# Performance work log

Hardware: AMD Instinct MI355X
Metric: run time of the kernel (lower is better)

The kernel has to match this reference:

```python
import jax, jax.numpy as jnp
import numpy as np
import math

B, N, M, C, H = 8, 2048, 2048, 512, 8
DK = C // H
EPS_LN = 1e-5


def _layernorm(x, g, b):
    mu = jnp.mean(x, axis=-1, keepdims=True)
    var = jnp.var(x, axis=-1, keepdims=True)
    return (x - mu) / jnp.sqrt(var + EPS_LN) * g + b


def setup_inputs() -> dict:
    key = jax.random.key(0)
    ks = jax.random.split(key, 8)
    s = 0.02
    return {
        "cross_x": jax.random.normal(ks[0], (B, N, C), jnp.float32),
        "cross_y": jax.random.normal(ks[1], (B, M, C), jnp.float32),
        "ln_x_g": jnp.ones((C,), jnp.float32),
        "ln_x_b": jnp.zeros((C,), jnp.float32),
        "ln_y_g": jnp.ones((C,), jnp.float32),
        "ln_y_b": jnp.zeros((C,), jnp.float32),
        "Wq": jax.random.normal(ks[2], (C, C), jnp.float32) * s,
        "bq": jnp.zeros((C,), jnp.float32),
        "Wk": jax.random.normal(ks[3], (C, C), jnp.float32) * s,
        "bk": jnp.zeros((C,), jnp.float32),
        "Wv": jax.random.normal(ks[4], (C, C), jnp.float32) * s,
        "bv": jnp.zeros((C,), jnp.float32),
        "Wc": jax.random.normal(ks[5], (C, C), jnp.float32) * s,  # conv1x1 weight [out, in]
        "bc": jnp.zeros((C,), jnp.float32),
        "ln_o_g": jnp.ones((C,), jnp.float32),
        "ln_o_b": jnp.zeros((C,), jnp.float32),
    }


def reference(cross_x, cross_y, ln_x_g, ln_x_b, ln_y_g, ln_y_b,
              Wq, bq, Wk, bk, Wv, bv, Wc, bc, ln_o_g, ln_o_b):
    b, n, c = cross_x.shape
    m = cross_y.shape[1]
    xn = _layernorm(cross_x, ln_x_g, ln_x_b)
    yn = _layernorm(cross_y, ln_y_g, ln_y_b)
    # projections -> [B, H, seq, dk]
    q = (xn @ Wq + bq).reshape(b, n, H, DK).transpose(0, 2, 1, 3)
    k = (yn @ Wk + bk).reshape(b, m, H, DK).transpose(0, 2, 1, 3)
    v = (yn @ Wv + bv).reshape(b, m, H, DK).transpose(0, 2, 1, 3)
    scale = 1.0 / math.sqrt(DK)
    scores = jnp.einsum("bhnd,bhmd->bhnm", q, k) * scale
    attn = jax.nn.softmax(scores, axis=-1)
    # extra renormalization across the HEAD dimension (dim=1)
    attn = attn / (1e-9 + jnp.sum(attn, axis=1, keepdims=True))
    # dropout is identity in eval/reference mode
    o = jnp.einsum("bhnm,bhmd->bhnd", attn, v)
    q_flat = q.transpose(0, 2, 1, 3).reshape(b, n, c)  # [B, N, C]
    o_flat = o.transpose(0, 2, 1, 3).reshape(b, n, c)
    # conv1x1 over channels on (query - x)
    h = (q_flat - o_flat) @ Wc.T + bc
    h = jax.nn.leaky_relu(_layernorm(h, ln_o_g, ln_o_b), negative_slope=0.02)
    return q_flat + h
```

## Files before the change

### kernel.cpp

```cpp
#include <hip/hip_runtime.h>


typedef short bf16x8 __attribute__((ext_vector_type(8)));
typedef float f32x4 __attribute__((ext_vector_type(4)));

#define CS 0.18033688f

#define BARRIER_LG() do { __builtin_amdgcn_sched_barrier(0); \
  asm volatile("s_waitcnt lgkmcnt(0)" ::: "memory"); \
  __builtin_amdgcn_s_barrier(); \
  __builtin_amdgcn_sched_barrier(0); } while(0)

#define VMCNT(N) do { __builtin_amdgcn_sched_barrier(0); \
  asm volatile("s_waitcnt vmcnt(" #N ")" ::: "memory"); \
  __builtin_amdgcn_sched_barrier(0); } while(0)

__device__ inline float b2f(unsigned short u){
  union { unsigned int i; float f; } c; c.i = ((unsigned int)u) << 16; return c.f;
}
__device__ inline unsigned short f2b(float f){
  union { float ff; unsigned int i; } c; c.ff = f;
  unsigned int i = c.i;
  return (unsigned short)((i + 0x7FFFu + ((i >> 16) & 1u)) >> 16);
}
__device__ inline unsigned int cvtpk(float lo, float hi){
  unsigned int r;
  asm("v_cvt_pk_bf16_f32 %0, %1, %2" : "=v"(r) : "v"(lo), "v"(hi));
  return r;
}
__device__ inline float fast_rcp(float x){ return __builtin_amdgcn_rcpf(x); }
__device__ inline f32x4 mfma16(bf16x8 a, bf16x8 b, f32x4 c){
  return __builtin_amdgcn_mfma_f32_16x16x32_bf16(a, b, c, 0, 0, 0);
}
__device__ __forceinline__ void gl16(const unsigned short* g, unsigned short* l){
  __builtin_amdgcn_global_load_lds(
      (const __attribute__((address_space(1))) unsigned int*)g,
      (__attribute__((address_space(3))) unsigned int*)l,
      16, 0, 0);
}

__global__ void detect_dtype(const unsigned int* __restrict__ g, int* __restrict__ flag){
  *flag = (g[0] == 0x3F800000u) ? 1 : 0;
}

__global__ void zero_f32(float* __restrict__ p, int n){
  int i = blockIdx.x * 256 + threadIdx.x;
  if (i < n) p[i] = 0.0f;
}

__global__ void convert_misc(const void* Wc, const void* bq, const void* bk,
    const void* bv, const void* bc, const void* go, const void* bo,
    unsigned short* WcB, unsigned short* bqB, unsigned short* bkB,
    unsigned short* bvB, unsigned short* bcB, unsigned short* goB,
    unsigned short* boB, const int* __restrict__ flag){
  int i = blockIdx.x * 256 + threadIdx.x;
  const void* src; unsigned short* dst; int o;
  if (i < 262144){ src = Wc; dst = WcB; o = i; }
  else {
    int j = i - 262144; int seg = j >> 9; o = j & 511;
    if (seg == 0){ src = bq; dst = bqB; }
    else if (seg == 1){ src = bk; dst = bkB; }
    else if (seg == 2){ src = bv; dst = bvB; }
    else if (seg == 3){ src = bc; dst = bcB; }
    else if (seg == 4){ src = go; dst = goB; }
    else if (seg == 5){ src = bo; dst = boB; }
    else return;
  }
  if (*flag) dst[o] = f2b(((const float*)src)[o]);
  else       dst[o] = ((const unsigned short*)src)[o];
}

__global__ __launch_bounds__(128) void ln_rows(const void* __restrict__ xv,
    const void* __restrict__ gxv, const void* __restrict__ bxv,
    const void* __restrict__ yv, const void* __restrict__ gyv, const void* __restrict__ byv,
    unsigned short* __restrict__ outx, unsigned short* __restrict__ outy,
    const int* __restrict__ flag){
  int row = blockIdx.x & 16383;
  int sel = blockIdx.x >> 14;
  const void* src = sel ? yv : xv;
  const void* gv = sel ? gyv : gxv;
  const void* bv_ = sel ? byv : bxv;
  unsigned short* out = sel ? outy : outx;
  int t = threadIdx.x;
  float v0, v1, v2, v3, g0, g1, g2, g3, bb0, bb1, bb2, bb3;
  if (*flag){
    float4 xf = ((const float4*)((const float*)src + (size_t)row * 512))[t];
    v0 = xf.x; v1 = xf.y; v2 = xf.z; v3 = xf.w;
    float4 gf = ((const float4*)gv)[t];  g0 = gf.x; g1 = gf.y; g2 = gf.z; g3 = gf.w;
    float4 bf = ((const float4*)bv_)[t]; bb0 = bf.x; bb1 = bf.y; bb2 = bf.z; bb3 = bf.w;
  } else {
    ushort4 raw = ((const ushort4*)((const unsigned short*)src + (size_t)row * 512))[t];
    v0 = b2f(raw.x); v1 = b2f(raw.y); v2 = b2f(raw.z); v3 = b2f(raw.w);
    ushort4 gr = ((const ushort4*)gv)[t];  g0 = b2f(gr.x); g1 = b2f(gr.y); g2 = b2f(gr.z); g3 = b2f(gr.w);
    ushort4 br = ((const ushort4*)bv_)[t]; bb0 = b2f(br.x); bb1 = b2f(br.y); bb2 = b2f(br.z); bb3 = b2f(br.w);
  }
  float s = v0 + v1 + v2 + v3;
  float sq = v0*v0 + v1*v1 + v2*v2 + v3*v3;
  #pragma unroll
  for (int off = 32; off; off >>= 1){
    s += __shfl_down(s, off, 64);
    sq += __shfl_down(sq, off, 64);
  }
  __shared__ float red[4];
  if ((t & 63) == 0){ red[(t >> 6)*2] = s; red[(t >> 6)*2 + 1] = sq; }
  __syncthreads();
  s = red[0] + red[2]; sq = red[1] + red[3];
  float mu = s * (1.0f/512.0f);
  float rstd = rsqrtf(sq * (1.0f/512.0f) - mu*mu + 1e-5f);
  ushort4 o;
  o.x = f2b((v0 - mu)*rstd*g0 + bb0);
  o.y = f2b((v1 - mu)*rstd*g1 + bb1);
  o.z = f2b((v2 - mu)*rstd*g2 + bb2);
  o.w = f2b((v3 - mu)*rstd*g3 + bb3);
  ((ushort4*)(out + (size_t)row * 512))[t] = o;
}

__global__ __launch_bounds__(256) void transposeW(const void* __restrict__ wq,
    const void* __restrict__ wk, const void* __restrict__ wv,
    unsigned short* __restrict__ oq, unsigned short* __restrict__ ok,
    unsigned short* __restrict__ ov, const int* __restrict__ flag){
  __shared__ unsigned short tile[32][33];
  const void* in = (blockIdx.z == 0) ? wq : (blockIdx.z == 1) ? wk : wv;
  unsigned short* outp = (blockIdx.z == 0) ? oq : (blockIdx.z == 1) ? ok : ov;
  int k0 = blockIdx.x * 32, j0 = blockIdx.y * 32;
  int t = threadIdx.x;
  int r = t >> 3, c4 = (t & 7) * 4;
  if (*flag){
    float4 v = *(const float4*)((const float*)in + (size_t)(k0 + r) * 512 + j0 + c4);
    tile[r][c4] = f2b(v.x); tile[r][c4+1] = f2b(v.y);
    tile[r][c4+2] = f2b(v.z); tile[r][c4+3] = f2b(v.w);
  } else {
    ushort4 v = *(const ushort4*)((const unsigned short*)in + (size_t)(k0 + r) * 512 + j0 + c4);
    tile[r][c4] = v.x; tile[r][c4+1] = v.y; tile[r][c4+2] = v.z; tile[r][c4+3] = v.w;
  }
  __syncthreads();
  ushort4 o;
  o.x = tile[c4][r]; o.y = tile[c4+1][r]; o.z = tile[c4+2][r]; o.w = tile[c4+3][r];
  *(ushort4*)(outp + (size_t)(j0 + r) * 512 + k0 + c4) = o;
}

template<int OUT_MODE>
__global__ __launch_bounds__(256) void gemm_nt(const unsigned short* __restrict__ A,
    const unsigned short* __restrict__ Bt, const unsigned short* __restrict__ bias,
    void* __restrict__ Cout){
  __shared__ __align__(16) unsigned short As[128*32];
  __shared__ __align__(16) unsigned short Bs[128*32];
  int i0 = blockIdx.x * 128;
  int j0 = blockIdx.y * 128;
  int t = threadIdx.x;
  int w = t >> 6, lane = t & 63;
  int quad = lane >> 4, l15 = lane & 15;
  int wrow = (w >> 1) * 64, wcol = (w & 1) * 64;
  f32x4 acc[4][4];
  #pragma unroll
  for (int a = 0; a < 4; a++)
    #pragma unroll
    for (int b = 0; b < 4; b++)
      acc[a][b] = (f32x4){0.f, 0.f, 0.f, 0.f};

  int ra0 = t >> 2, ca0 = (t & 3) * 8;
  const unsigned short* Ag = A + (size_t)i0 * 512;
  const unsigned short* Bg = Bt + (size_t)j0 * 512;

  for (int kt = 0; kt < 16; kt++){
    int k0 = kt * 32;
    int4 av0 = *(const int4*)(Ag + (size_t)ra0 * 512 + k0 + ca0);
    int4 av1 = *(const int4*)(Ag + (size_t)(64 + ra0) * 512 + k0 + ca0);
    int4 bv0 = *(const int4*)(Bg + (size_t)ra0 * 512 + k0 + ca0);
    int4 bv1 = *(const int4*)(Bg + (size_t)(64 + ra0) * 512 + k0 + ca0);
    __syncthreads();
    ((int4*)As)[t] = av0; ((int4*)As)[t + 256] = av1;
    ((int4*)Bs)[t] = bv0; ((int4*)Bs)[t + 256] = bv1;
    __syncthreads();
    bf16x8 af[4], bfg[4];
    #pragma unroll
    for (int a = 0; a < 4; a++)
      af[a] = *(const bf16x8*)&As[(wrow + a*16 + l15)*32 + quad*8];
    #pragma unroll
    for (int b = 0; b < 4; b++)
      bfg[b] = *(const bf16x8*)&Bs[(wcol + b*16 + l15)*32 + quad*8];
    #pragma unroll
    for (int a = 0; a < 4; a++)
      #pragma unroll
      for (int b = 0; b < 4; b++)
        acc[a][b] = mfma16(af[a], bfg[b], acc[a][b]);
  }

  #pragma unroll
  for (int b = 0; b < 4; b++){
    int gcol = j0 + wcol + b*16 + l15;
    float bv = b2f(bias[gcol]);
    #pragma unroll
    for (int a = 0; a < 4; a++){
      #pragma unroll
      for (int r = 0; r < 4; r++){
        int grow = i0 + wrow + a*16 + quad*4 + r;
        float v = acc[a][b][r] + bv;
        if (OUT_MODE == 0){
          ((unsigned short*)Cout)[(size_t)grow*512 + gcol] = f2b(v);
        } else {
          int bb_ = grow >> 11, m = grow & 2047;
          int h = gcol >> 6, d = gcol & 63;
          ((unsigned short*)Cout)[(((size_t)(bb_*64 + (m >> 5))*512) + h*64 + d)*32
                                  + (m & 31)] = f2b(v);
        }
      }
    }
  }
}

__global__ __launch_bounds__(256) void attn_lsum(const unsigned short* __restrict__ Qm,
    const unsigned short* __restrict__ Km, float* __restrict__ Lsum){
  int wgl = blockIdx.x * 4 + (threadIdx.x >> 6);
  int b = wgl >> 9; int r_ = wgl & 511;
  int ntl = r_ >> 4; int ms = (r_ >> 2) & 3; int hg = r_ & 3;
  int h0 = hg * 2;
  int lane = threadIdx.x & 63, quad = lane >> 4, l15 = lane & 15;
  int n0 = ntl * 64;
  const unsigned short* Kp = Km + ((size_t)(b*2048)) * 512;
  bf16x8 aq[4][2][2];
  #pragma unroll
  for (int ns = 0; ns < 4; ns++)
    #pragma unroll
    for (int hh = 0; hh < 2; hh++)
      #pragma unroll
      for (int ks = 0; ks < 2; ks++)
        aq[ns][hh][ks] = *(const bf16x8*)(Qm + ((size_t)(b*2048 + n0 + ns*16 + l15))*512
                                          + (h0+hh)*64 + ks*32 + quad*8);
  float ls[4][2];
  #pragma unroll
  for (int ns = 0; ns < 4; ns++){ ls[ns][0] = 0.f; ls[ns][1] = 0.f; }
  for (int mt = 0; mt < 16; mt++){
    int m0 = ms*512 + mt*32;
    #pragma unroll
    for (int msub = 0; msub < 2; msub++){
      int mb = m0 + msub*16;
      #pragma unroll
      for (int hh = 0; hh < 2; hh++){
        bf16x8 ak0 = *(const bf16x8*)(Kp + (size_t)(mb + l15)*512 + (h0+hh)*64 + quad*8);
        bf16x8 ak1 = *(const bf16x8*)(Kp + (size_t)(mb + l15)*512 + (h0+hh)*64 + 32 + quad*8);
        #pragma unroll
        for (int ns = 0; ns < 4; ns++){
          f32x4 S = (f32x4){0.f,0.f,0.f,0.f};
          S = mfma16(ak0, aq[ns][hh][0], S);
          S = mfma16(ak1, aq[ns][hh][1], S);
          float e0 = exp2f(S[0]*CS), e1 = exp2f(S[1]*CS);
          float e2 = exp2f(S[2]*CS), e3 = exp2f(S[3]*CS);
          ls[ns][hh] += (e0 + e1) + (e2 + e3);
        }
      }
    }
  }
  #pragma unroll
  for (int ns = 0; ns < 4; ns++)
    #pragma unroll
    for (int hh = 0; hh < 2; hh++){
      float v = ls[ns][hh];
      v += __shfl_xor(v, 16, 64);
      v += __shfl_xor(v, 32, 64);
      ls[ns][hh] = v;
    }
  if (lane < 16){
    #pragma unroll
    for (int ns = 0; ns < 4; ns++)
      #pragma unroll
      for (int hh = 0; hh < 2; hh++)
        atomicAdd(&Lsum[(size_t)(b*8 + h0 + hh)*2048 + n0 + ns*16 + lane], ls[ns][hh]);
  }
}

__global__ __launch_bounds__(1024)
__attribute__((amdgpu_waves_per_eu(4, 4)))
void attn_out(const unsigned short* __restrict__ Qm,
    const unsigned short* __restrict__ Km, const unsigned short* __restrict__ VTm,
    const float* __restrict__ Lsum, unsigned short* __restrict__ DQO){
  __shared__ __align__(16) unsigned short Ks[32*512];
  __shared__ __align__(16) unsigned short Vs[512*32];
  __shared__ __align__(16) float ps[4*4*16*36];
  __shared__ __align__(16) unsigned short pbv[4*4*2*16*40];
  int bid = blockIdx.x;
  int b = bid & 7;
  int ntl = bid >> 3;
  int t = threadIdx.x;
  int w = t >> 6;
  int hp = w & 3;
  int nsub = w >> 2;
  int lane = t & 63, quad = lane >> 4, l15 = lane & 15;
  int h0 = hp * 2;
  int n0 = ntl * 64 + nsub * 16;
  int kx = (l15 & 7) << 4;
  int vx = (quad ^ (l15 & 3)) << 4;

  const unsigned short* Kg = Km + (size_t)b * 1048576;
  const unsigned short* Vg = VTm + (size_t)b * 1048576;
  const unsigned short* Qp = Qm + ((size_t)(b*2048 + n0)) * 512;

  bf16x8 aq[2][2];
  #pragma unroll
  for (int hh = 0; hh < 2; hh++)
    #pragma unroll
    for (int ks = 0; ks < 2; ks++)
      aq[hh][ks] = *(const bf16x8*)(Qp + (size_t)l15*512 + (h0+hh)*64 + ks*32 + quad*8);
  float lg[2];
  #pragma unroll
  for (int hh = 0; hh < 2; hh++)
    lg[hh] = -log2f(Lsum[(size_t)(b*8 + h0 + hh)*2048 + n0 + l15]);
  f32x4 oacc[2][4];
  #pragma unroll
  for (int hh = 0; hh < 2; hh++)
    #pragma unroll
    for (int d = 0; d < 4; d++)
      oacc[hh][d] = (f32x4){0.f,0.f,0.f,0.f};

  int ksl = (lane ^ (w & 7)) << 3;
  unsigned short* kd0 = Ks + (w << 9);
  unsigned short* kd1 = Ks + ((w + 16) << 9);
  unsigned short* vd0 = Vs + t*8;
  unsigned short* vd1 = Vs + t*8 + 8192;
  int vsrc_off = (t >> 2)*32 + (((t & 3) ^ ((t >> 2) & 3)) << 3);

  float* psn = ps + nsub * 2304;
  float* pso = psn + hp * 576 + l15 * 36;
  unsigned short* pbn = pbv + nsub * 5120 + hp * 1280;

  gl16(Kg + ((size_t)(w     ) << 9) + ksl, kd0);
  gl16(Kg + ((size_t)(w + 16) << 9) + ksl, kd1);
  gl16(Vg + vsrc_off, vd0);
  gl16(Vg + vsrc_off + 8192, vd1);

  for (int mt = 0; mt < 64; mt++){
    VMCNT(2);
    BARRIER_LG();
    float p[2][2][4];
    f32x4 s_own[2];
    #pragma unroll
    for (int msub = 0; msub < 2; msub++){
      const char* kr = (const char*)Ks + ((msub*16 + l15) << 10);
      #pragma unroll
      for (int hh = 0; hh < 2; hh++){
        int cb = (h0 + hh) * 128;
        bf16x8 k0 = *(const bf16x8*)(kr + ((cb + quad*16) ^ kx));
        bf16x8 k1 = *(const bf16x8*)(kr + ((cb + 64 + quad*16) ^ kx));
        f32x4 S = (f32x4){0.f,0.f,0.f,0.f};
        S = mfma16(k0, aq[hh][0], S);
        S = mfma16(k1, aq[hh][1], S);
        #pragma unroll
        for (int r = 0; r < 4; r++) p[hh][msub][r] = exp2f(fmaf(S[r], CS, lg[hh]));
      }
      f32x4 so;
      #pragma unroll
      for (int r = 0; r < 4; r++) so[r] = p[0][msub][r] + p[1][msub][r];
      s_own[msub] = so;
      *(f32x4*)(pso + msub*16 + quad*4) = so;
    }
    VMCNT(0);
    BARRIER_LG();
    if (mt < 63){
      const unsigned short* Kt = Kg + ((size_t)(mt+1) << 14);
      gl16(Kt + ((size_t)(w     ) << 9) + ksl, kd0);
      gl16(Kt + ((size_t)(w + 16) << 9) + ksl, kd1);
    }
    f32x4 ir4[2];
    #pragma unroll
    for (int msub = 0; msub < 2; msub++){
      f32x4 tt = s_own[msub];
      #pragma unroll
      for (int j = 1; j < 4; j++){
        int hq = (hp + j) & 3;
        tt += *(const f32x4*)(psn + hq*576 + l15*36 + msub*16 + quad*4);
      }
      f32x4 ir;
      #pragma unroll
      for (int r = 0; r < 4; r++) ir[r] = fast_rcp(1e-9f + tt[r]);
      ir4[msub] = ir;
    }
    #pragma unroll
    for (int hh = 0; hh < 2; hh++){
      #pragma unroll
      for (int msub = 0; msub < 2; msub++){
        int2 pv;
        pv.x = (int)cvtpk(p[hh][msub][0]*ir4[msub][0], p[hh][msub][1]*ir4[msub][1]);
        pv.y = (int)cvtpk(p[hh][msub][2]*ir4[msub][2], p[hh][msub][3]*ir4[msub][3]);
        *(int2*)&pbn[(hh*16 + l15)*40 + msub*16 + quad*4] = pv;
      }
    }
    #pragma unroll
    for (int hh = 0; hh < 2; hh++){
      bf16x8 wp = *(const bf16x8*)((const char*)pbn + (hh*16 + l15)*80 + quad*16);
      const char* vb = (const char*)Vs + (((h0+hh)*64 + l15) << 6) + vx;
      #pragma unroll
      for (int d = 0; d < 4; d++){
        bf16x8 vv = *(const bf16x8*)(vb + (d << 10));
        oacc[hh][d] = mfma16(vv, wp, oacc[hh][d]);
      }
    }
    BARRIER_LG();
    if (mt < 63){
      const unsigned short* Vt = Vg + ((size_t)(mt+1) << 14);
      gl16(Vt + vsrc_off, vd0);
      gl16(Vt + vsrc_off + 8192, vd1);
    }
  }
  {
    size_t nrow = (size_t)(b*2048 + n0 + l15);
    const unsigned short* Qrow = Qm + nrow * 512;
    unsigned short* Drow = DQO + nrow * 512;
    #pragma unroll
    for (int hh = 0; hh < 2; hh++){
      #pragma unroll
      for (int d = 0; d < 4; d++){
        int c = (h0+hh)*64 + d*16 + quad*4;
        ushort4 qv = *(const ushort4*)(Qrow + c);
        ushort4 ov;
        ov.x = f2b(b2f(qv.x) - oacc[hh][d][0]);
        ov.y = f2b(b2f(qv.y) - oacc[hh][d][1]);
        ov.z = f2b(b2f(qv.z) - oacc[hh][d][2]);
        ov.w = f2b(b2f(qv.w) - oacc[hh][d][3]);
        *(ushort4*)(Drow + c) = ov;
      }
    }
  }
}

__global__ __launch_bounds__(128) void finalize_k(const unsigned short* __restrict__ H,
    const unsigned short* __restrict__ Qb, const unsigned short* __restrict__ g,
    const unsigned short* __restrict__ bb, void* __restrict__ outp,
    const int* __restrict__ flag){
  int row = blockIdx.x; int t = threadIdx.x;
  ushort4 hraw = ((const ushort4*)(H + (size_t)row * 512))[t];
  float h0 = b2f(hraw.x), h1 = b2f(hraw.y), h2 = b2f(hraw.z), h3 = b2f(hraw.w);
  float s = h0 + h1 + h2 + h3;
  float sq = h0*h0 + h1*h1 + h2*h2 + h3*h3;
  #pragma unroll
  for (int off = 32; off; off >>= 1){
    s += __shfl_down(s, off, 64);
    sq += __shfl_down(sq, off, 64);
  }
  __shared__ float red[4];
  if ((t & 63) == 0){ red[(t >> 6)*2] = s; red[(t >> 6)*2 + 1] = sq; }
  __syncthreads();
  s = red[0] + red[2]; sq = red[1] + red[3];
  float mu = s * (1.0f/512.0f);
  float rstd = rsqrtf(sq * (1.0f/512.0f) - mu*mu + 1e-5f);
  ushort4 gr = ((const ushort4*)g)[t];
  ushort4 br = ((const ushort4*)bb)[t];
  ushort4 qr = ((const ushort4*)(Qb + (size_t)row * 512))[t];
  float y0 = (h0 - mu)*rstd*b2f(gr.x) + b2f(br.x); y0 = fmaxf(y0, 0.02f*y0);
  float y1 = (h1 - mu)*rstd*b2f(gr.y) + b2f(br.y); y1 = fmaxf(y1, 0.02f*y1);
  float y2 = (h2 - mu)*rstd*b2f(gr.z) + b2f(br.z); y2 = fmaxf(y2, 0.02f*y2);
  float y3 = (h3 - mu)*rstd*b2f(gr.w) + b2f(br.w); y3 = fmaxf(y3, 0.02f*y3);
  float o0 = b2f(qr.x) + y0, o1 = b2f(qr.y) + y1, o2 = b2f(qr.z) + y2, o3 = b2f(qr.w) + y3;
  if (*flag){
    float4 o; o.x = o0; o.y = o1; o.z = o2; o.w = o3;
    ((float4*)((float*)outp + (size_t)row * 512))[t] = o;
  } else {
    ushort4 o; o.x = f2b(o0); o.y = f2b(o1); o.z = f2b(o2); o.w = f2b(o3);
    ((ushort4*)((unsigned short*)outp + (size_t)row * 512))[t] = o;
  }
}

extern "C" void kernel_launch(void* const* d_in, const int* in_sizes, int n_in,
                              void* d_out, int out_size, void* d_ws, size_t ws_size,
                              hipStream_t stream){
  const void* x      = d_in[0];
  const void* y      = d_in[1];
  const void* ln_x_g = d_in[2];
  const void* ln_x_b = d_in[3];
  const void* ln_y_g = d_in[4];
  const void* ln_y_b = d_in[5];
  const void* Wq     = d_in[6];
  const void* bq     = d_in[7];
  const void* Wk     = d_in[8];
  const void* bk     = d_in[9];
  const void* Wv     = d_in[10];
  const void* bv     = d_in[11];
  const void* Wc     = d_in[12];
  const void* bc     = d_in[13];
  const void* ln_o_g = d_in[14];
  const void* ln_o_b = d_in[15];

  const size_t MB = (size_t)1 << 20;
  char* ws = (char*)d_ws;
  unsigned short* Qb  = (unsigned short*)(ws);
  unsigned short* Kb  = (unsigned short*)(ws + 16*MB);
  unsigned short* VT  = (unsigned short*)(ws + 32*MB);
  unsigned short* XN  = (unsigned short*)(ws + 48*MB);
  unsigned short* YN  = (unsigned short*)(ws + 64*MB);
  unsigned short* DQO = XN;
  unsigned short* Hpre = YN;
  unsigned short* WqT = (unsigned short*)(ws + 80*MB);
  unsigned short* WkT = WqT + 512*512;
  unsigned short* WvT = WkT + 512*512;
  unsigned short* WcB = WvT + 512*512;
  unsigned short* bqB = (unsigned short*)(ws + 82*MB);
  unsigned short* bkB = bqB + 512;
  unsigned short* bvB = bkB + 512;
  unsigned short* bcB = bvB + 512;
  unsigned short* goB = bcB + 512;
  unsigned short* boB = goB + 512;
  float* Lsum         = (float*)(ws + 83*MB);
  int* Flag           = (int*)(ws + 84*MB);

  detect_dtype<<<dim3(1), dim3(1), 0, stream>>>((const unsigned int*)ln_x_g, Flag);
  zero_f32<<<dim3(512), dim3(256), 0, stream>>>(Lsum, 131072);
  convert_misc<<<dim3(1037), dim3(256), 0, stream>>>(Wc, bq, bk, bv, bc, ln_o_g, ln_o_b,
      WcB, bqB, bkB, bvB, bcB, goB, boB, Flag);
  ln_rows<<<dim3(32768), dim3(128), 0, stream>>>(x, ln_x_g, ln_x_b, y, ln_y_g, ln_y_b,
      XN, YN, Flag);
  transposeW<<<dim3(16,16,3), dim3(256), 0, stream>>>(Wq, Wk, Wv, WqT, WkT, WvT, Flag);
  gemm_nt<0><<<dim3(128,4), dim3(256), 0, stream>>>(XN, WqT, bqB, (void*)Qb);
  gemm_nt<0><<<dim3(128,4), dim3(256), 0, stream>>>(YN, WkT, bkB, (void*)Kb);
  gemm_nt<2><<<dim3(128,4), dim3(256), 0, stream>>>(YN, WvT, bvB, (void*)VT);
  attn_lsum<<<dim3(1024), dim3(256), 0, stream>>>(Qb, Kb, Lsum);
  attn_out<<<dim3(256), dim3(1024), 0, stream>>>(Qb, Kb, VT, Lsum, DQO);
  gemm_nt<0><<<dim3(128,4), dim3(256), 0, stream>>>(DQO, WcB, bcB, (void*)Hpre);
  finalize_k<<<dim3(16384), dim3(128), 0, stream>>>(Hpre, Qb, goB, boB, d_out, Flag);
}
```

Measured before the change: 519.8 us.

## Double-buffer GEMM LDS tiles with direct global-to-LDS async loads

The projection GEMM kernel now uses two LDS buffers per operand and a gl16 direct global-to-LDS load helper to prefetch the next K-tile while MFMAs run on the current one. This removes the register round-trip and one of the two barriers per iteration, overlapping memory latency with compute. LDS use doubles, which could lower occupancy. Each iteration still waits on vmcnt(0) before its barrier, so the overlap is limited to one tile ahead.

```diff
diff --git a/kernel.cpp b/kernel.cpp
--- a/kernel.cpp
+++ b/kernel.cpp
@@ -143,8 +143,8 @@
 __global__ __launch_bounds__(256) void gemm_nt(const unsigned short* __restrict__ A,
     const unsigned short* __restrict__ Bt, const unsigned short* __restrict__ bias,
     void* __restrict__ Cout){
-  __shared__ __align__(16) unsigned short As[128*32];
-  __shared__ __align__(16) unsigned short Bs[128*32];
+  __shared__ __align__(16) unsigned short As[2][128*32];
+  __shared__ __align__(16) unsigned short Bs[2][128*32];
   int i0 = blockIdx.x * 128;
   int j0 = blockIdx.y * 128;
   int t = threadIdx.x;
@@ -159,26 +159,36 @@
       acc[a][b] = (f32x4){0.f, 0.f, 0.f, 0.f};
 
   int ra0 = t >> 2, ca0 = (t & 3) * 8;
-  const unsigned short* Ag = A + (size_t)i0 * 512;
-  const unsigned short* Bg = Bt + (size_t)j0 * 512;
+  const unsigned short* Ag = A + (size_t)(i0 + ra0) * 512 + ca0;
+  const unsigned short* Bg = Bt + (size_t)(j0 + ra0) * 512 + ca0;
+  unsigned short* ad0[2] = { As[0] + t*8, As[1] + t*8 };
+  unsigned short* bd0[2] = { Bs[0] + t*8, Bs[1] + t*8 };
+
+  gl16(Ag, ad0[0]);
+  gl16(Ag + 64*512, ad0[0] + 2048);
+  gl16(Bg, bd0[0]);
+  gl16(Bg + 64*512, bd0[0] + 2048);
 
   for (int kt = 0; kt < 16; kt++){
-    int k0 = kt * 32;
-    int4 av0 = *(const int4*)(Ag + (size_t)ra0 * 512 + k0 + ca0);
-    int4 av1 = *(const int4*)(Ag + (size_t)(64 + ra0) * 512 + k0 + ca0);
-    int4 bv0 = *(const int4*)(Bg + (size_t)ra0 * 512 + k0 + ca0);
-    int4 bv1 = *(const int4*)(Bg + (size_t)(64 + ra0) * 512 + k0 + ca0);
-    __syncthreads();
-    ((int4*)As)[t] = av0; ((int4*)As)[t + 256] = av1;
-    ((int4*)Bs)[t] = bv0; ((int4*)Bs)[t + 256] = bv1;
-    __syncthreads();
+    int cur = kt & 1;
+    VMCNT(0);
+    BARRIER_LG();
+    if (kt < 15){
+      int ko = (kt + 1) * 32;
+      gl16(Ag + ko, ad0[cur ^ 1]);
+      gl16(Ag + ko + 64*512, ad0[cur ^ 1] + 2048);
+      gl16(Bg + ko, bd0[cur ^ 1]);
+      gl16(Bg + ko + 64*512, bd0[cur ^ 1] + 2048);
+    }
+    const unsigned short* Ac = As[cur];
+    const unsigned short* Bc = Bs[cur];
     bf16x8 af[4], bfg[4];
     #pragma unroll
     for (int a = 0; a < 4; a++)
-      af[a] = *(const bf16x8*)&As[(wrow + a*16 + l15)*32 + quad*8];
+      af[a] = *(const bf16x8*)&Ac[(wrow + a*16 + l15)*32 + quad*8];
     #pragma unroll
     for (int b = 0; b < 4; b++)
-      bfg[b] = *(const bf16x8*)&Bs[(wcol + b*16 + l15)*32 + quad*8];
+      bfg[b] = *(const bf16x8*)&Bc[(wcol + b*16 + l15)*32 + quad*8];
     #pragma unroll
     for (int a = 0; a < 4; a++)
       #pragma unroll
```

New measurement: 522.7 us. No clear change (+0.6%).
